# Kernel optimization log

Measured on AMD Instinct MI355X. Metric: run time of the kernel, lower is better.

The kernel has to match this reference:

```python
import jax, jax.numpy as jnp
import numpy as np

B, N, F, E = 2, 50000, 128, 500000


def setup_inputs() -> dict:
    key = jax.random.key(0)
    ks = jax.random.split(key, 7)
    x0 = jax.random.normal(ks[0], (B, N, F), dtype=jnp.float32)
    dst = jax.random.randint(ks[1], (E,), 0, N, dtype=jnp.int32)
    src = jax.random.randint(ks[2], (E,), 0, N, dtype=jnp.int32)
    # torch Linear weights: [out_features, in_features]
    w0 = jax.random.normal(ks[3], (F, 2 * F), dtype=jnp.float32) * 0.05
    b0 = jax.random.normal(ks[4], (F,), dtype=jnp.float32) * 0.05
    w1 = jax.random.normal(ks[5], (F, F), dtype=jnp.float32) * 0.05
    b1 = jax.random.normal(ks[6], (F,), dtype=jnp.float32) * 0.05
    return {"x0": x0, "dst": dst, "src": src, "w0": w0, "b0": b0, "w1": w1, "b1": b1}


def reference(x0, dst, src, w0, b0, w1, b1):
    n = x0.shape[1]
    # gather source node features per edge: [B, E, F] -> [E, B, F] for segment ops
    xe = jnp.transpose(x0[:, src], (1, 0, 2))
    # scatter-reduce over destination nodes (include_self=False semantics)
    s = jax.ops.segment_sum(xe, dst, num_segments=n)                      # [N, B, F]
    mx = jax.ops.segment_max(xe, dst, num_segments=n)                     # [N, B, F]
    cnt = jax.ops.segment_sum(jnp.ones((dst.shape[0],), x0.dtype), dst, num_segments=n)  # [N]
    has_edge = (cnt > 0)[:, None, None]
    x0t = jnp.transpose(x0, (1, 0, 2))                                    # [N, B, F]
    # nodes with no incoming edges keep their original values
    mean = jnp.where(has_edge, s / jnp.maximum(cnt, 1.0)[:, None, None], x0t)
    amax = jnp.where(has_edge, mx, x0t)
    x = jnp.concatenate([mean, amax], axis=-1)                            # [N, B, 2F]
    h = jax.nn.relu(jnp.einsum('nbf,of->nbo', x, w0) + b0)
    # dropout is identity in eval mode
    out = x0t + jnp.einsum('nbf,of->nbo', h, w1) + b1
    return jnp.transpose(out, (1, 0, 2))                                  # [B, N, F]
```

## Files before the change

kernel.cpp:

```cpp
#include <hip/hip_runtime.h>

#define NN 50000
#define FF 128
constexpr int NBF2 = NN * 256;
constexpr int CAP  = 64;

typedef __attribute__((ext_vector_type(4))) short short4v;
typedef __attribute__((ext_vector_type(8))) short short8;
typedef __attribute__((ext_vector_type(4))) float floatx4;

__device__ __forceinline__ unsigned short f2bf(float x) {
    unsigned int u = __float_as_uint(x);
    unsigned int r = (u + 0x7fff + ((u >> 16) & 1)) >> 16;
    return (unsigned short)r;
}
__device__ __forceinline__ float bf2f(short x) {
    return __uint_as_float(((unsigned int)(unsigned short)x) << 16);
}

__global__ __launch_bounds__(256)
void convert_fill(const int* __restrict__ dst, const int* __restrict__ src, int E,
                  const float* __restrict__ x0,
                  const float* __restrict__ w0, const float* __restrict__ w1,
                  int* __restrict__ cursor, int* __restrict__ esrc,
                  unsigned short* __restrict__ x0b,
                  unsigned short* __restrict__ w0b, unsigned short* __restrict__ w1b) {
    int i = blockIdx.x * 256 + threadIdx.x;
    if (i < E) {
        int d = dst[i];
        int pos = atomicAdd(&cursor[d], 1);
        if (pos < CAP) esrc[d * CAP + pos] = src[i];
    }
    int stride = gridDim.x * 256;
    for (int p = i; p < NBF2 / 4; p += stride) {
        int v0 = p * 4;
        int n = v0 >> 8;
        int b = (v0 >> 7) & 1;
        int f = v0 & 127;
        const float4 in = *(const float4*)&x0[(b * NN + n) * FF + f];
        short4v o = { (short)f2bf(in.x), (short)f2bf(in.y), (short)f2bf(in.z), (short)f2bf(in.w) };
        *(short4v*)&x0b[v0] = o;
    }
    if (i < 128 * 256) w0b[i] = f2bf(w0[i]);
    if (i < 128 * 128) w1b[i] = f2bf(w1[i]);
}

constexpr int NPB = 16;
constexpr int XCP = 256 + 8;
constexpr int HSP = 128 + 8;

__global__ __launch_bounds__(256, 4)
void fused_gcn(const unsigned short* __restrict__ x0b,
               const float* __restrict__ x0,
               const int* __restrict__ deg,
               const int* __restrict__ esrc,
               const unsigned short* __restrict__ w0b,
               const float* __restrict__ b0,
               const unsigned short* __restrict__ w1b,
               const float* __restrict__ b1,
               float* __restrict__ out) {
    __shared__ unsigned short xc[32 * XCP];
    __shared__ int sl_hs[32 * HSP / 2];
    __shared__ int cum[17];
    int* sl = sl_hs;
    unsigned short* hs = (unsigned short*)sl_hs;

    int t = threadIdx.x;
    int q = t >> 6;
    int l = t & 63;
    int n0 = blockIdx.x * NPB;

    if (t < 16) cum[t + 1] = min(deg[n0 + t], CAP);
    if (t == 16) cum[0] = 0;
    __syncthreads();
    if (t == 0) {
        int run = 0;
        for (int i = 1; i <= 16; ++i) { run += cum[i]; cum[i] = run; }
    }
    __syncthreads();

    int T = cum[16];
    for (int i = t; i < T + 8; i += 256) {
        if (i < T) {
            int j = 0;
            while (cum[j + 1] <= i) ++j;
            sl[i] = (j << 16) | esrc[(n0 + j) * CAP + (i - cum[j])];
        } else {
            sl[i] = (16 << 16) | 0xFFFF;
        }
    }
    __syncthreads();

    int l4 = l * 4;
    int bb = l >> 5;
    int ff = (l & 31) * 4;
    const float NEG_INF = __int_as_float(0xFF800000);

    int jb = q * 4;
    int nb = n0 + jb;
    int eS = __builtin_amdgcn_readfirstlane(cum[jb]);
    int eE = __builtin_amdgcn_readfirstlane(cum[jb + 4]);

    float sA0=0,sA1=0,sA2=0,sA3=0, sB0=0,sB1=0,sB2=0,sB3=0;
    float sC0=0,sC1=0,sC2=0,sC3=0, sD0=0,sD1=0,sD2=0,sD3=0;
    float mA0=NEG_INF,mA1=NEG_INF,mA2=NEG_INF,mA3=NEG_INF;
    float mB0=NEG_INF,mB1=NEG_INF,mB2=NEG_INF,mB3=NEG_INF;
    float mC0=NEG_INF,mC1=NEG_INF,mC2=NEG_INF,mC3=NEG_INF;
    float mD0=NEG_INF,mD1=NEG_INF,mD2=NEG_INF,mD3=NEG_INF;

#define GATH_K(k) \
    int u##k = __builtin_amdgcn_readfirstlane(sl[e + k]); \
    short4v r##k = *(const short4v*)&x0b[(unsigned)(u##k & 0xffff) * 256 + l4];

#define ACC_K(k) { \
    int ja = u##k >> 16; \
    if ((ja >> 2) == q) { \
        float v0=bf2f(r##k[0]), v1=bf2f(r##k[1]), v2=bf2f(r##k[2]), v3=bf2f(r##k[3]); \
        int g = ja & 3; \
        if (g == 0)      { sA0+=v0;sA1+=v1;sA2+=v2;sA3+=v3; mA0=fmaxf(mA0,v0);mA1=fmaxf(mA1,v1);mA2=fmaxf(mA2,v2);mA3=fmaxf(mA3,v3); } \
        else if (g == 1) { sB0+=v0;sB1+=v1;sB2+=v2;sB3+=v3; mB0=fmaxf(mB0,v0);mB1=fmaxf(mB1,v1);mB2=fmaxf(mB2,v2);mB3=fmaxf(mB3,v3); } \
        else if (g == 2) { sC0+=v0;sC1+=v1;sC2+=v2;sC3+=v3; mC0=fmaxf(mC0,v0);mC1=fmaxf(mC1,v1);mC2=fmaxf(mC2,v2);mC3=fmaxf(mC3,v3); } \
        else             { sD0+=v0;sD1+=v1;sD2+=v2;sD3+=v3; mD0=fmaxf(mD0,v0);mD1=fmaxf(mD1,v1);mD2=fmaxf(mD2,v2);mD3=fmaxf(mD3,v3); } \
    } }

    for (int e = eS; e < eE; e += 8) {
        GATH_K(0) GATH_K(1) GATH_K(2) GATH_K(3)
        GATH_K(4) GATH_K(5) GATH_K(6) GATH_K(7)
        ACC_K(0) ACC_K(1) ACC_K(2) ACC_K(3)
        ACC_K(4) ACC_K(5) ACC_K(6) ACC_K(7)
    }
#undef GATH_K
#undef ACC_K

#define FINAL_G(g, S0,S1,S2,S3, M0,M1,M2,M3) { \
    int dgx = __builtin_amdgcn_readfirstlane(cum[jb + g + 1] - cum[jb + g]); \
    float me0,me1,me2,me3,a0,a1,a2,a3; \
    if (dgx > 0) { \
        float inv = 1.0f / (float)dgx; \
        me0=S0*inv; me1=S1*inv; me2=S2*inv; me3=S3*inv; \
        a0=M0; a1=M1; a2=M2; a3=M3; \
    } else { \
        short4v rr = *(const short4v*)&x0b[(nb + g) * 256 + l4]; \
        me0=a0=bf2f(rr[0]); me1=a1=bf2f(rr[1]); me2=a2=bf2f(rr[2]); me3=a3=bf2f(rr[3]); \
    } \
    int row = (jb + g) * 2 + bb; \
    short4v mv = { (short)f2bf(me0),(short)f2bf(me1),(short)f2bf(me2),(short)f2bf(me3) }; \
    short4v av = { (short)f2bf(a0),(short)f2bf(a1),(short)f2bf(a2),(short)f2bf(a3) }; \
    *(short4v*)&xc[row * XCP + ff]       = mv; \
    *(short4v*)&xc[row * XCP + 128 + ff] = av; \
}
    FINAL_G(0, sA0,sA1,sA2,sA3, mA0,mA1,mA2,mA3)
    FINAL_G(1, sB0,sB1,sB2,sB3, mB0,mB1,mB2,mB3)
    FINAL_G(2, sC0,sC1,sC2,sC3, mC0,mC1,mC2,mC3)
    FINAL_G(3, sD0,sD1,sD2,sD3, mD0,mD1,mD2,mD3)
#undef FINAL_G
    __syncthreads();

    int m    = l & 15;
    int quad = l >> 4;
    int rowbase = (q >> 1) * 16;
    int colbase = (q & 1) * 64;

    floatx4 acc[4];
#pragma unroll
    for (int ct = 0; ct < 4; ++ct) acc[ct] = (floatx4){0.f, 0.f, 0.f, 0.f};
#pragma unroll
    for (int ks = 0; ks < 8; ++ks) {
        short8 a = *(const short8*)&xc[(rowbase + m) * XCP + ks * 32 + quad * 8];
#pragma unroll
        for (int ct = 0; ct < 4; ++ct) {
            short8 bf = *(const short8*)&w0b[(colbase + ct * 16 + m) * 256 + ks * 32 + quad * 8];
            acc[ct] = __builtin_amdgcn_mfma_f32_16x16x32_bf16(a, bf, acc[ct], 0, 0, 0);
        }
    }
#pragma unroll
    for (int ct = 0; ct < 4; ++ct) {
        int col = colbase + ct * 16 + m;
        float bias = b0[col];
#pragma unroll
        for (int r = 0; r < 4; ++r) {
            int row = rowbase + quad * 4 + r;
            hs[row * HSP + col] = f2bf(fmaxf(acc[ct][r] + bias, 0.0f));
        }
    }
    __syncthreads();

    floatx4 acc2[4];
#pragma unroll
    for (int ct = 0; ct < 4; ++ct) acc2[ct] = (floatx4){0.f, 0.f, 0.f, 0.f};
#pragma unroll
    for (int ks = 0; ks < 4; ++ks) {
        short8 a = *(const short8*)&hs[(rowbase + m) * HSP + ks * 32 + quad * 8];
#pragma unroll
        for (int ct = 0; ct < 4; ++ct) {
            short8 bf = *(const short8*)&w1b[(colbase + ct * 16 + m) * 128 + ks * 32 + quad * 8];
            acc2[ct] = __builtin_amdgcn_mfma_f32_16x16x32_bf16(a, bf, acc2[ct], 0, 0, 0);
        }
    }
#pragma unroll
    for (int ct = 0; ct < 4; ++ct) {
        int col = colbase + ct * 16 + m;
        float bias = b1[col];
#pragma unroll
        for (int r = 0; r < 4; ++r) {
            int row = rowbase + quad * 4 + r;
            int n  = n0 + (row >> 1);
            int b2 = row & 1;
            int oi = (b2 * NN + n) * FF + col;
            out[oi] = x0[oi] + bias + acc2[ct][r];
        }
    }
}

extern "C" void kernel_launch(void* const* d_in, const int* in_sizes, int n_in,
                              void* d_out, int out_size, void* d_ws, size_t ws_size,
                              hipStream_t stream) {
    const float* x0  = (const float*)d_in[0];
    const int*   dst = (const int*)d_in[1];
    const int*   src = (const int*)d_in[2];
    const float* w0  = (const float*)d_in[3];
    const float* b0  = (const float*)d_in[4];
    const float* w1  = (const float*)d_in[5];
    const float* b1  = (const float*)d_in[6];
    float* out = (float*)d_out;
    int E = in_sizes[1];

    int* cursor = (int*)d_ws;
    int* esrc   = cursor + NN;
    unsigned short* x0b = (unsigned short*)(esrc + (size_t)NN * CAP);
    unsigned short* w0b = x0b + NBF2;
    unsigned short* w1b = w0b + 128 * 256;

    int eb = (E + 255) / 256;

    hipMemsetAsync(cursor, 0, (size_t)NN * sizeof(int), stream);
    convert_fill<<<eb, 256, 0, stream>>>(dst, src, E, x0, w0, w1, cursor, esrc, x0b, w0b, w1b);
    fused_gcn<<<NN / NPB, 256, 0, stream>>>(x0b, x0, cursor, esrc, w0b, b0, w1b, b1, out);
}
```

Before: 246.6 us.

## Split fused GCN into separate gather-reduce and MLP kernels with feature slicing

Replaces the single fused gather-plus-MLP kernel with two kernels. The first is a gather_reduce kernel that slices features across blocks and has 8-lane groups process edges in parallel, with shuffle reductions. It writes the concatenated mean/max rows to a bf16 global buffer. The second is an MLP kernel that loads those rows into shared memory and runs both MFMA matmuls. Edge fill and x0 conversion also become separate kernels, and the residual add now reads the bf16 copy of x0 instead of the fp32 original. This aims to improve load balance and parallelism in the gather. In exchange it adds an extra global round trip for the intermediate buffer and loses precision in the residual.

```diff
diff --git a/kernel.cpp b/kernel.cpp
--- a/kernel.cpp
+++ b/kernel.cpp
@@ -18,19 +18,21 @@
     return __uint_as_float(((unsigned int)(unsigned short)x) << 16);
 }
 
-__global__ __launch_bounds__(256)
-void convert_fill(const int* __restrict__ dst, const int* __restrict__ src, int E,
-                  const float* __restrict__ x0,
-                  const float* __restrict__ w0, const float* __restrict__ w1,
-                  int* __restrict__ cursor, int* __restrict__ esrc,
-                  unsigned short* __restrict__ x0b,
-                  unsigned short* __restrict__ w0b, unsigned short* __restrict__ w1b) {
+__global__ void fill_edges(const int* __restrict__ dst, const int* __restrict__ src,
+                           int E, int* __restrict__ cursor, int* __restrict__ esrc) {
+    int stride = gridDim.x * blockDim.x;
+    for (int e = blockIdx.x * blockDim.x + threadIdx.x; e < E; e += stride) {
+        int d = dst[e];
+        int pos = atomicAdd(&cursor[d], 1);
+        if (pos < CAP) esrc[d * CAP + pos] = src[e];
+    }
+}
+
+__global__ void convert_x(const float* __restrict__ x0,
+                          const float* __restrict__ w0, const float* __restrict__ w1,
+                          unsigned short* __restrict__ x0b,
+                          unsigned short* __restrict__ w0b, unsigned short* __restrict__ w1b) {
     int i = blockIdx.x * 256 + threadIdx.x;
-    if (i < E) {
-        int d = dst[i];
-        int pos = atomicAdd(&cursor[d], 1);
-        if (pos < CAP) esrc[d * CAP + pos] = src[i];
-    }
     int stride = gridDim.x * 256;
     for (int p = i; p < NBF2 / 4; p += stride) {
         int v0 = p * 4;
@@ -45,115 +47,95 @@
     if (i < 128 * 128) w1b[i] = f2bf(w1[i]);
 }
 
+constexpr int GNPB = 40;
+
+__global__ __launch_bounds__(256)
+void gather_reduce(const unsigned short* __restrict__ x0b,
+                   const int* __restrict__ deg,
+                   const int* __restrict__ esrc,
+                   unsigned short* __restrict__ xcg) {
+    int slice = blockIdx.x & 7;
+    int chunk = blockIdx.x >> 3;
+    int t = threadIdx.x;
+    int q = t >> 6;
+    int l = t & 63;
+    int g  = l >> 3;
+    int li = l & 7;
+    int fo  = slice * 32 + li * 4;
+    int bs  = slice >> 2;
+    int f0s = (slice & 3) * 32;
+    const float NEG_INF = __int_as_float(0xFF800000);
+
+    int n = chunk * GNPB + q * (GNPB / 4);
+    for (int j = 0; j < GNPB / 4; ++j, ++n) {
+        int dg = min(deg[n], CAP);
+        int nbase = n * CAP;
+        float s0 = 0.f, s1 = 0.f, s2 = 0.f, s3 = 0.f;
+        float m0 = NEG_INF, m1 = NEG_INF, m2 = NEG_INF, m3 = NEG_INF;
+        for (int e = 0; e < dg; e += 8) {
+            int ee = e + g;
+            bool valid = ee < dg;
+            int idx = esrc[nbase + (valid ? ee : 0)];
+            short4v r = *(const short4v*)&x0b[(unsigned)idx * 256 + fo];
+            float v0 = bf2f(r[0]), v1 = bf2f(r[1]), v2 = bf2f(r[2]), v3 = bf2f(r[3]);
+            if (valid) {
+                s0 += v0; s1 += v1; s2 += v2; s3 += v3;
+                m0 = fmaxf(m0, v0); m1 = fmaxf(m1, v1);
+                m2 = fmaxf(m2, v2); m3 = fmaxf(m3, v3);
+            }
+        }
+#pragma unroll
+        for (int off = 8; off <= 32; off <<= 1) {
+            s0 += __shfl_xor(s0, off); s1 += __shfl_xor(s1, off);
+            s2 += __shfl_xor(s2, off); s3 += __shfl_xor(s3, off);
+            m0 = fmaxf(m0, __shfl_xor(m0, off)); m1 = fmaxf(m1, __shfl_xor(m1, off));
+            m2 = fmaxf(m2, __shfl_xor(m2, off)); m3 = fmaxf(m3, __shfl_xor(m3, off));
+        }
+        float me0, me1, me2, me3, a0, a1, a2, a3;
+        if (dg > 0) {
+            float inv = 1.0f / (float)dg;
+            me0 = s0 * inv; me1 = s1 * inv; me2 = s2 * inv; me3 = s3 * inv;
+            a0 = m0; a1 = m1; a2 = m2; a3 = m3;
+        } else {
+            short4v rr = *(const short4v*)&x0b[n * 256 + fo];
+            me0 = a0 = bf2f(rr[0]); me1 = a1 = bf2f(rr[1]);
+            me2 = a2 = bf2f(rr[2]); me3 = a3 = bf2f(rr[3]);
+        }
+        if (l < 8) {
+            short4v mv = { (short)f2bf(me0), (short)f2bf(me1), (short)f2bf(me2), (short)f2bf(me3) };
+            short4v av = { (short)f2bf(a0), (short)f2bf(a1), (short)f2bf(a2), (short)f2bf(a3) };
+            unsigned base = (unsigned)n * 512 + bs * 256 + f0s + li * 4;
+            *(short4v*)&xcg[base]       = mv;
+            *(short4v*)&xcg[base + 128] = av;
+        }
+    }
+}
+
 constexpr int NPB = 16;
 constexpr int XCP = 256 + 8;
 constexpr int HSP = 128 + 8;
 
-__global__ __launch_bounds__(256, 4)
-void fused_gcn(const unsigned short* __restrict__ x0b,
-               const float* __restrict__ x0,
-               const int* __restrict__ deg,
-               const int* __restrict__ esrc,
-               const unsigned short* __restrict__ w0b,
-               const float* __restrict__ b0,
-               const unsigned short* __restrict__ w1b,
-               const float* __restrict__ b1,
-               float* __restrict__ out) {
+__global__ __launch_bounds__(256)
+void mlp(const unsigned short* __restrict__ xcg,
+         const unsigned short* __restrict__ x0b,
+         const unsigned short* __restrict__ w0b,
+         const float* __restrict__ b0,
+         const unsigned short* __restrict__ w1b,
+         const float* __restrict__ b1,
+         float* __restrict__ out) {
     __shared__ unsigned short xc[32 * XCP];
-    __shared__ int sl_hs[32 * HSP / 2];
-    __shared__ int cum[17];
-    int* sl = sl_hs;
-    unsigned short* hs = (unsigned short*)sl_hs;
+    __shared__ unsigned short hs[32 * HSP];
 
     int t = threadIdx.x;
     int q = t >> 6;
     int l = t & 63;
     int n0 = blockIdx.x * NPB;
 
-    if (t < 16) cum[t + 1] = min(deg[n0 + t], CAP);
-    if (t == 16) cum[0] = 0;
-    __syncthreads();
-    if (t == 0) {
-        int run = 0;
-        for (int i = 1; i <= 16; ++i) { run += cum[i]; cum[i] = run; }
-    }
-    __syncthreads();
-
-    int T = cum[16];
-    for (int i = t; i < T + 8; i += 256) {
-        if (i < T) {
-            int j = 0;
-            while (cum[j + 1] <= i) ++j;
-            sl[i] = (j << 16) | esrc[(n0 + j) * CAP + (i - cum[j])];
-        } else {
-            sl[i] = (16 << 16) | 0xFFFF;
-        }
-    }
-    __syncthreads();
-
-    int l4 = l * 4;
-    int bb = l >> 5;
-    int ff = (l & 31) * 4;
-    const float NEG_INF = __int_as_float(0xFF800000);
-
-    int jb = q * 4;
-    int nb = n0 + jb;
-    int eS = __builtin_amdgcn_readfirstlane(cum[jb]);
-    int eE = __builtin_amdgcn_readfirstlane(cum[jb + 4]);
-
-    float sA0=0,sA1=0,sA2=0,sA3=0, sB0=0,sB1=0,sB2=0,sB3=0;
-    float sC0=0,sC1=0,sC2=0,sC3=0, sD0=0,sD1=0,sD2=0,sD3=0;
-    float mA0=NEG_INF,mA1=NEG_INF,mA2=NEG_INF,mA3=NEG_INF;
-    float mB0=NEG_INF,mB1=NEG_INF,mB2=NEG_INF,mB3=NEG_INF;
-    float mC0=NEG_INF,mC1=NEG_INF,mC2=NEG_INF,mC3=NEG_INF;
-    float mD0=NEG_INF,mD1=NEG_INF,mD2=NEG_INF,mD3=NEG_INF;
-
-#define GATH_K(k) \
-    int u##k = __builtin_amdgcn_readfirstlane(sl[e + k]); \
-    short4v r##k = *(const short4v*)&x0b[(unsigned)(u##k & 0xffff) * 256 + l4];
-
-#define ACC_K(k) { \
-    int ja = u##k >> 16; \
-    if ((ja >> 2) == q) { \
-        float v0=bf2f(r##k[0]), v1=bf2f(r##k[1]), v2=bf2f(r##k[2]), v3=bf2f(r##k[3]); \
-        int g = ja & 3; \
-        if (g == 0)      { sA0+=v0;sA1+=v1;sA2+=v2;sA3+=v3; mA0=fmaxf(mA0,v0);mA1=fmaxf(mA1,v1);mA2=fmaxf(mA2,v2);mA3=fmaxf(mA3,v3); } \
-        else if (g == 1) { sB0+=v0;sB1+=v1;sB2+=v2;sB3+=v3; mB0=fmaxf(mB0,v0);mB1=fmaxf(mB1,v1);mB2=fmaxf(mB2,v2);mB3=fmaxf(mB3,v3); } \
-        else if (g == 2) { sC0+=v0;sC1+=v1;sC2+=v2;sC3+=v3; mC0=fmaxf(mC0,v0);mC1=fmaxf(mC1,v1);mC2=fmaxf(mC2,v2);mC3=fmaxf(mC3,v3); } \
-        else             { sD0+=v0;sD1+=v1;sD2+=v2;sD3+=v3; mD0=fmaxf(mD0,v0);mD1=fmaxf(mD1,v1);mD2=fmaxf(mD2,v2);mD3=fmaxf(mD3,v3); } \
-    } }
-
-    for (int e = eS; e < eE; e += 8) {
-        GATH_K(0) GATH_K(1) GATH_K(2) GATH_K(3)
-        GATH_K(4) GATH_K(5) GATH_K(6) GATH_K(7)
-        ACC_K(0) ACC_K(1) ACC_K(2) ACC_K(3)
-        ACC_K(4) ACC_K(5) ACC_K(6) ACC_K(7)
-    }
-#undef GATH_K
-#undef ACC_K
-
-#define FINAL_G(g, S0,S1,S2,S3, M0,M1,M2,M3) { \
-    int dgx = __builtin_amdgcn_readfirstlane(cum[jb + g + 1] - cum[jb + g]); \
-    float me0,me1,me2,me3,a0,a1,a2,a3; \
-    if (dgx > 0) { \
-        float inv = 1.0f / (float)dgx; \
-        me0=S0*inv; me1=S1*inv; me2=S2*inv; me3=S3*inv; \
-        a0=M0; a1=M1; a2=M2; a3=M3; \
-    } else { \
-        short4v rr = *(const short4v*)&x0b[(nb + g) * 256 + l4]; \
-        me0=a0=bf2f(rr[0]); me1=a1=bf2f(rr[1]); me2=a2=bf2f(rr[2]); me3=a3=bf2f(rr[3]); \
-    } \
-    int row = (jb + g) * 2 + bb; \
-    short4v mv = { (short)f2bf(me0),(short)f2bf(me1),(short)f2bf(me2),(short)f2bf(me3) }; \
-    short4v av = { (short)f2bf(a0),(short)f2bf(a1),(short)f2bf(a2),(short)f2bf(a3) }; \
-    *(short4v*)&xc[row * XCP + ff]       = mv; \
-    *(short4v*)&xc[row * XCP + 128 + ff] = av; \
-}
-    FINAL_G(0, sA0,sA1,sA2,sA3, mA0,mA1,mA2,mA3)
-    FINAL_G(1, sB0,sB1,sB2,sB3, mB0,mB1,mB2,mB3)
-    FINAL_G(2, sC0,sC1,sC2,sC3, mC0,mC1,mC2,mC3)
-    FINAL_G(3, sD0,sD1,sD2,sD3, mD0,mD1,mD2,mD3)
-#undef FINAL_G
+    for (int i = t; i < 1024; i += 256) {
+        int row = i >> 5;
+        int col = (i & 31) * 8;
+        *(short8*)&xc[row * XCP + col] = *(const short8*)&xcg[(unsigned)n0 * 512 + i * 8];
+    }
     __syncthreads();
 
     int m    = l & 15;
@@ -206,8 +188,8 @@
             int row = rowbase + quad * 4 + r;
             int n  = n0 + (row >> 1);
             int b2 = row & 1;
-            int oi = (b2 * NN + n) * FF + col;
-            out[oi] = x0[oi] + bias + acc2[ct][r];
+            float res = bf2f((short)x0b[(unsigned)n * 256 + b2 * 128 + col]);
+            out[(b2 * NN + n) * FF + col] = res + bias + acc2[ct][r];
         }
     }
 }
@@ -228,12 +210,13 @@
     int* cursor = (int*)d_ws;
     int* esrc   = cursor + NN;
     unsigned short* x0b = (unsigned short*)(esrc + (size_t)NN * CAP);
-    unsigned short* w0b = x0b + NBF2;
+    unsigned short* xcg = x0b + NBF2;
+    unsigned short* w0b = xcg + (size_t)NN * 512;
     unsigned short* w1b = w0b + 128 * 256;
 
-    int eb = (E + 255) / 256;
-
     hipMemsetAsync(cursor, 0, (size_t)NN * sizeof(int), stream);
-    convert_fill<<<eb, 256, 0, stream>>>(dst, src, E, x0, w0, w1, cursor, esrc, x0b, w0b, w1b);
-    fused_gcn<<<NN / NPB, 256, 0, stream>>>(x0b, x0, cursor, esrc, w0b, b0, w1b, b1, out);
-}
+    fill_edges<<<2048, 256, 0, stream>>>(dst, src, E, cursor, esrc);
+    convert_x<<<4096, 256, 0, stream>>>(x0, w0, w1, x0b, w0b, w1b);
+    gather_reduce<<<(NN / GNPB) * 8, 256, 0, stream>>>(x0b, cursor, esrc, xcg);
+    mlp<<<NN / NPB, 256, 0, stream>>>(xcg, x0b, w0b, b0, w1b, b1, out);
+}
```

After: 359.3 us. 45.7% more time.
